# Kernel tuning notes

Hardware: AMD Instinct MI355X
Metric: run time of the kernel (lower is better)

The kernel has to match this reference:

```python
import jax, jax.numpy as jnp
import numpy as np

# dims: batch, seq, model dim, heads, head_k_dim, head_v_dim, conv size
B, S, D, H, DK, DV, K = 1, 2048, 1024, 8, 128, 128, 4
KD, VD = H * DK, H * DV  # key_dim, value_dim


def _silu(x):
    return x * jax.nn.sigmoid(x)


def _l2norm(x, eps=1e-6):
    return x * jax.lax.rsqrt(jnp.sum(x * x, -1, keepdims=True) + eps)


def _causal_conv_silu(x, w):
    # depthwise causal conv1d (ShortConvolution, activation='silu', no bias)
    # x: [b, s, d], w: [d, K]
    Kc = w.shape[1]
    xp = jnp.pad(x, ((0, 0), (Kc - 1, 0), (0, 0)))
    y = sum(xp[:, i:i + x.shape[1], :] * w[:, i] for i in range(Kc))
    return _silu(y)


def _rmsnorm(x, w, eps=1e-5):
    return x * jax.lax.rsqrt(jnp.mean(x * x, -1, keepdims=True) + eps) * w


def _kda(q, k, v, g, beta):
    # gated delta-rule linear attention (KDA), recurrent form == chunk_kda math
    # q,k,g: [B,S,H,DK]; v: [B,S,H,DV]; beta: [B,S,H]
    scale = DK ** -0.5
    qn = _l2norm(q) * scale  # use_qk_l2norm_in_kernel=True
    kn = _l2norm(k)

    def step(Sm, inp):
        q_t, k_t, v_t, g_t, b_t = inp  # [B,H,DK], [B,H,DK], [B,H,DV], [B,H,DK], [B,H]
        Sm = Sm * jnp.exp(g_t)[..., None]                    # per-key-channel decay
        v_new = (v_t - jnp.einsum('bhk,bhkv->bhv', k_t, Sm)) * b_t[..., None]
        Sm = Sm + k_t[..., None] * v_new[..., None, :]       # delta-rule update
        o_t = jnp.einsum('bhk,bhkv->bhv', q_t, Sm)
        return Sm, o_t

    xs = (jnp.swapaxes(qn, 0, 1), jnp.swapaxes(kn, 0, 1), jnp.swapaxes(v, 0, 1),
          jnp.swapaxes(g, 0, 1), jnp.swapaxes(beta, 0, 1))
    S0 = jnp.zeros((q.shape[0], H, DK, DV), jnp.float32)
    _, o = jax.lax.scan(step, S0, xs)
    return jnp.swapaxes(o, 0, 1)  # [B,S,H,DV]


def setup_inputs() -> dict:
    key = jax.random.key(0)
    ks = jax.random.split(key, 20)

    def w(k, shape, fan_in):
        return jax.random.normal(k, shape, jnp.float32) / np.sqrt(fan_in)

    return {
        'x': jax.random.normal(ks[0], (B, S, D), jnp.float32),
        've': jax.random.normal(ks[1], (B, S, D), jnp.float32),
        'sa_lambdas': jax.random.uniform(ks[2], (2,), jnp.float32),
        'Wq': w(ks[3], (KD, D), D), 'Wk': w(ks[4], (KD, D), D), 'Wv': w(ks[5], (VD, D), D),
        'Wo': w(ks[6], (D, VD), VD),
        'wq_conv': w(ks[7], (KD, K), K), 'wk_conv': w(ks[8], (KD, K), K), 'wv_conv': w(ks[9], (VD, K), K),
        'Wf1': w(ks[10], (DV, D), D), 'Wf2': w(ks[11], (KD, DV), DV),
        'Wb': w(ks[12], (H, D), D),
        'A_log': jnp.log(jax.random.uniform(ks[13], (H,), jnp.float32, 1.0, 16.0)),
        'dt_bias': jnp.zeros((KD,), jnp.float32),
        'Wg1': w(ks[14], (DV, D), D), 'Wg2': w(ks[15], (VD, DV), DV),
        'bg2': jnp.zeros((VD,), jnp.float32),
        'w_norm': jnp.ones((DV,), jnp.float32),
    }


def reference(x, ve, sa_lambdas, Wq, Wk, Wv, Wo, wq_conv, wk_conv, wv_conv,
              Wf1, Wf2, Wb, A_log, dt_bias, Wg1, Wg2, bg2, w_norm):
    b, s, _ = x.shape
    # q/k/v projections + short causal conv with silu
    q = _causal_conv_silu(x @ Wq.T, wq_conv)
    k = _causal_conv_silu(x @ Wk.T, wk_conv)
    v = _causal_conv_silu(x @ Wv.T, wv_conv)
    # fused_kda_gate: g = -exp(A_log) * softplus(f_proj(x) + dt_bias), per [H, DK]
    g = (x @ Wf1.T) @ Wf2.T
    g = jax.nn.softplus((g + dt_bias).astype(jnp.float32)).reshape(b, s, H, DK)
    g = -jnp.exp(A_log)[None, None, :, None] * g
    beta = jax.nn.sigmoid((x @ Wb.T).astype(jnp.float32))  # [b,s,H]
    q = q.reshape(b, s, H, DK)
    k = k.reshape(b, s, H, DK)
    v = v.reshape(b, s, H, DV)
    # mix v with value-embedding ve (3-D branch of _mix_v_with_ve)
    ve_v = _causal_conv_silu(ve @ Wv.T, wv_conv).reshape(b, s, H, DV)
    v = sa_lambdas[0] * v + sa_lambdas[1] * ve_v
    o = _kda(q, k, v, g, beta)  # [b,s,H,DV]
    # FusedRMSNormGated(activation='sigmoid'): rmsnorm(o)*w then gate
    g_out = ((x @ Wg1.T) @ Wg2.T + bg2).reshape(b, s, H, DV)
    o = _rmsnorm(o, w_norm) * jax.nn.sigmoid(g_out)
    return o.reshape(b, s, VD) @ Wo.T
```

## Files before the change

kernel.cpp:

```cpp
#include <hip/hip_runtime.h>
#include <math.h>
#include <stdint.h>

#define S_LEN 2048
#define DMODEL 1024
#define NH 8
#define DK_ 128
#define DV_ 128
#define KD_ 1024
#define KCONV 4
#define CW 32
#define NW2 64
#define PREB_STRIDE 17408
#define TKH_OFF 0
#define QHT_OFF 4096
#define KCT_OFF 8192
#define TV_OFF 12288
#define NN_OFF 16384
#define RS 164
#define GS 20

typedef short bf16x8 __attribute__((ext_vector_type(8)));
typedef float f32x4 __attribute__((ext_vector_type(4)));

__device__ __forceinline__ uint16_t f2bf(float f) {
  uint32_t u = __float_as_uint(f);
  u += 0x7FFF + ((u >> 16) & 1);
  return (uint16_t)(u >> 16);
}
__device__ __forceinline__ float bf2f(uint16_t u) {
  return __uint_as_float((uint32_t)u << 16);
}
__device__ __forceinline__ void glds16(const uint16_t* g, uint16_t* l) {
  __builtin_amdgcn_global_load_lds(
      (const __attribute__((address_space(1))) void*)g,
      (__attribute__((address_space(3))) void*)l, 16, 0, 0);
}
__device__ __forceinline__ float dot4(float4 a, float4 b) {
  return fmaf(a.w, b.w, fmaf(a.z, b.z, fmaf(a.y, b.y, a.x * b.x)));
}
__device__ __forceinline__ float4 f4add(float4 a, float4 b) {
  float4 r; r.x = a.x + b.x; r.y = a.y + b.y; r.z = a.z + b.z; r.w = a.w + b.w; return r;
}
__device__ __forceinline__ float4 f4sub(float4 a, float4 b) {
  float4 r; r.x = a.x - b.x; r.y = a.y - b.y; r.z = a.z - b.z; r.w = a.w - b.w; return r;
}
__device__ __forceinline__ float4 f4mul(float4 a, float4 b) {
  float4 r; r.x = a.x * b.x; r.y = a.y * b.y; r.z = a.z * b.z; r.w = a.w * b.w; return r;
}
__device__ __forceinline__ float4 f4s(float4 a, float s) {
  float4 r; r.x = a.x * s; r.y = a.y * s; r.z = a.z * s; r.w = a.w * s; return r;
}
__device__ __forceinline__ float4 f4expc(float4 a) {
  float4 r;
  r.x = expf(fminf(a.x, 0.f)); r.y = expf(fminf(a.y, 0.f));
  r.z = expf(fminf(a.z, 0.f)); r.w = expf(fminf(a.w, 0.f));
  return r;
}
__device__ __forceinline__ float4 f4exp(float4 a) {
  float4 r; r.x = expf(a.x); r.y = expf(a.y); r.z = expf(a.z); r.w = expf(a.w); return r;
}
__device__ __forceinline__ uint4 pack8(float4 a, float4 b) {
  uint4 r;
  r.x = (uint32_t)f2bf(a.x) | ((uint32_t)f2bf(a.y) << 16);
  r.y = (uint32_t)f2bf(a.z) | ((uint32_t)f2bf(a.w) << 16);
  r.z = (uint32_t)f2bf(b.x) | ((uint32_t)f2bf(b.y) << 16);
  r.w = (uint32_t)f2bf(b.z) | ((uint32_t)f2bf(b.w) << 16);
  return r;
}
__device__ __forceinline__ uint2 pack4(f32x4 a) {
  uint2 r;
  r.x = (uint32_t)f2bf(a[0]) | ((uint32_t)f2bf(a[1]) << 16);
  r.y = (uint32_t)f2bf(a[2]) | ((uint32_t)f2bf(a[3]) << 16);
  return r;
}
union U4B8 { uint4 u; bf16x8 b; };
__device__ __forceinline__ bf16x8 u2b(uint4 u) { U4B8 x; x.u = u; return x.b; }

#define DPPADD(x, ctrl) \
  x += __int_as_float(__builtin_amdgcn_update_dpp(0, __float_as_int(x), ctrl, 0xF, 0xF, true))

__device__ __forceinline__ void row8_sum2(float& a, float& b) {
  DPPADD(a, 0xB1); DPPADD(b, 0xB1);
  DPPADD(a, 0x4E); DPPADD(b, 0x4E);
  DPPADD(a, 0x141); DPPADD(b, 0x141);
}
__device__ __forceinline__ void row8_arr8x2(float* x, float* y) {
#pragma unroll
  for (int i = 0; i < 8; i++) { DPPADD(x[i], 0xB1); DPPADD(y[i], 0xB1); }
#pragma unroll
  for (int i = 0; i < 8; i++) { DPPADD(x[i], 0x4E); DPPADD(y[i], 0x4E); }
#pragma unroll
  for (int i = 0; i < 8; i++) { DPPADD(x[i], 0x141); DPPADD(y[i], 0x141); }
}

struct CastArgs {
  const float* s[8];
  uint16_t* d[8];
  int n[8];
};
__global__ __launch_bounds__(256) void cast_multi(CastArgs a) {
  int i = blockIdx.y;
  const int step = gridDim.x * 256 * 8;
  for (int base = (blockIdx.x * 256 + threadIdx.x) * 8; base < a.n[i]; base += step) {
    const float4* sp = (const float4*)(a.s[i] + base);
    float4 x0 = sp[0], x1 = sp[1];
    *(uint4*)(a.d[i] + base) = pack8(x0, x1);
  }
}

__global__ __launch_bounds__(256) void gemm_wc(
    const float* __restrict__ A,
    const float* __restrict__ B,
    uint16_t* __restrict__ C) {
  __shared__ float As[16][68];
  __shared__ float Bs[16][68];
  const int tid = threadIdx.x;
  const int m0 = blockIdx.y * 64, n0 = blockIdx.x * 64;
  const int tx = tid & 15, ty = tid >> 4;
  const int lk = tid & 15, lr = tid >> 4;
  const int bc = tid & 63, bkr = tid >> 6;
  float acc[4][4] = {};
  for (int k0 = 0; k0 < 128; k0 += 16) {
#pragma unroll
    for (int i = 0; i < 4; i++) {
      As[lk][lr + 16 * i] = A[(size_t)(m0 + lr + 16 * i) * 128 + k0 + lk];
      Bs[bkr + 4 * i][bc] = B[(size_t)(k0 + bkr + 4 * i) * 1024 + n0 + bc];
    }
    __syncthreads();
#pragma unroll
    for (int kk = 0; kk < 16; kk++) {
      float4 a4 = *(const float4*)&As[kk][ty * 4];
      float4 b4 = *(const float4*)&Bs[kk][tx * 4];
      float av[4] = {a4.x, a4.y, a4.z, a4.w};
      float bv[4] = {b4.x, b4.y, b4.z, b4.w};
#pragma unroll
      for (int i = 0; i < 4; i++)
#pragma unroll
        for (int jx = 0; jx < 4; jx++) acc[i][jx] = fmaf(av[i], bv[jx], acc[i][jx]);
    }
    __syncthreads();
  }
#pragma unroll
  for (int i = 0; i < 4; i++)
#pragma unroll
    for (int jx = 0; jx < 4; jx++)
      C[(size_t)(m0 + ty * 4 + i) * 1024 + n0 + tx * 4 + jx] = f2bf(acc[i][jx]);
}

__global__ __launch_bounds__(256) void pad_wb(const float* __restrict__ Wb,
                                              uint16_t* __restrict__ Wbp) {
  int idx = blockIdx.x * 256 + threadIdx.x;
  if (idx >= 128 * 1024) return;
  int r = idx >> 10;
  Wbp[idx] = (r < 8) ? f2bf(Wb[idx]) : (uint16_t)0;
}

struct GJobs {
  const uint16_t* A[8];
  const uint16_t* B[8];
  void* C[8];
  int N[8];
  int outbf[8];
};
__global__ __launch_bounds__(256) void gemm_mfma(GJobs j, int K) {
  const int z = blockIdx.z;
  const int N = j.N[z];
  const int n0 = blockIdx.x * 128;
  if (n0 >= N) return;
  __shared__ uint16_t Asb[128 * 32];
  __shared__ uint16_t Bsb[128 * 32];
  const uint16_t* __restrict__ A = j.A[z];
  const uint16_t* __restrict__ B = j.B[z];
  const int tid = threadIdx.x;
  const int w = tid >> 6, lane = tid & 63;
  const int m0 = blockIdx.y * 128;
  const int mw = (w & 1) * 64, nw = (w >> 1) * 64;
  const int c0 = tid, c1 = 256 + tid;
  const int r0 = c0 >> 2, cl0 = (c0 & 3) ^ ((r0 >> 2) & 3);
  const int r1 = c1 >> 2, cl1 = (c1 & 3) ^ ((r1 >> 2) & 3);
  const uint16_t* gA0 = A + (size_t)(m0 + r0) * K + cl0 * 8;
  const uint16_t* gA1 = A + (size_t)(m0 + r1) * K + cl1 * 8;
  const uint16_t* gB0 = B + (size_t)(n0 + r0) * K + cl0 * 8;
  const uint16_t* gB1 = B + (size_t)(n0 + r1) * K + cl1 * 8;
  uint16_t* lA0 = Asb + w * 512;
  uint16_t* lA1 = Asb + 2048 + w * 512;
  uint16_t* lB0 = Bsb + w * 512;
  uint16_t* lB1 = Bsb + 2048 + w * 512;

  const int l15 = lane & 15, q = lane >> 4;
  const int ccq = q ^ ((l15 >> 2) & 3);

  f32x4 acc[4][4] = {};
  for (int k0 = 0; k0 < K; k0 += 32) {
    glds16(gA0 + k0, lA0);
    glds16(gA1 + k0, lA1);
    glds16(gB0 + k0, lB0);
    glds16(gB1 + k0, lB1);
    __syncthreads();
    bf16x8 af[4], bfr[4];
#pragma unroll
    for (int i = 0; i < 4; i++)
      af[i] = *(const bf16x8*)&Asb[(mw + i * 16 + l15) * 32 + ccq * 8];
#pragma unroll
    for (int jx = 0; jx < 4; jx++)
      bfr[jx] = *(const bf16x8*)&Bsb[(nw + jx * 16 + l15) * 32 + ccq * 8];
#pragma unroll
    for (int i = 0; i < 4; i++)
#pragma unroll
      for (int jx = 0; jx < 4; jx++)
        acc[i][jx] = __builtin_amdgcn_mfma_f32_16x16x32_bf16(af[i], bfr[jx],
                                                             acc[i][jx], 0, 0, 0);
    __syncthreads();
  }
  const int obf = j.outbf[z];
#pragma unroll
  for (int i = 0; i < 4; i++) {
#pragma unroll
    for (int jx = 0; jx < 4; jx++) {
      int n = n0 + nw + jx * 16 + l15;
#pragma unroll
      for (int r = 0; r < 4; r++) {
        int m = m0 + mw + i * 16 + q * 4 + r;
        if (obf)
          ((uint16_t*)j.C[z])[(size_t)m * N + n] = f2bf(acc[i][jx][r]);
        else
          ((float*)j.C[z])[(size_t)m * N + n] = acc[i][jx][r];
      }
    }
  }
}

__global__ __launch_bounds__(256) void conv_silu_mix(
    const uint16_t* __restrict__ qp, const uint16_t* __restrict__ kp,
    const uint16_t* __restrict__ vp, const uint16_t* __restrict__ vep,
    const float* __restrict__ wq, const float* __restrict__ wk,
    const float* __restrict__ wv, const float* __restrict__ lam,
    float* __restrict__ qc, float* __restrict__ kc, float* __restrict__ vmx) {
  int idx = blockIdx.x * 256 + threadIdx.x;
  if (idx >= S_LEN * KD_) return;
  int s = idx >> 10, d = idx & 1023;
  float aq = 0.f, ak = 0.f, av = 0.f, ae = 0.f;
#pragma unroll
  for (int i = 0; i < KCONV; i++) {
    int ss = s - (KCONV - 1) + i;
    if (ss < 0) continue;
    size_t off = (size_t)ss * KD_ + d;
    aq = fmaf(bf2f(qp[off]), wq[d * KCONV + i], aq);
    ak = fmaf(bf2f(kp[off]), wk[d * KCONV + i], ak);
    av = fmaf(bf2f(vp[off]), wv[d * KCONV + i], av);
    ae = fmaf(bf2f(vep[off]), wv[d * KCONV + i], ae);
  }
  qc[idx] = aq / (1.f + expf(-aq));
  kc[idx] = ak / (1.f + expf(-ak));
  float sv = av / (1.f + expf(-av));
  float se = ae / (1.f + expf(-ae));
  vmx[idx] = lam[0] * sv + lam[1] * se;
}

__global__ __launch_bounds__(256) void kda_pre(
    const float* __restrict__ qc, const float* __restrict__ kc,
    const float* __restrict__ graw, const float* __restrict__ vm,
    const float* __restrict__ bpre, const float* __restrict__ dt_bias,
    const float* __restrict__ A_log, uint16_t* __restrict__ preB,
    float* __restrict__ preF) {
  __shared__ float kls[32 * RS];
  __shared__ float Gls[32 * RS];
  __shared__ float Mcm[32 * 36];
  __shared__ float bls[32];
  const int w = blockIdx.x >> 3, h = blockIdx.x & 7;
  const int tid = threadIdx.x;
  const int t = tid >> 3, kq = tid & 7;
  const int wv = tid >> 6;
  const size_t gb = (size_t)blockIdx.x * PREB_STRIDE;
  const size_t gf = (size_t)blockIdx.x * 128;

  size_t roff = (size_t)(w * CW + t) * KD_ + h * DK_ + kq * 16;
  float4 kv[4], qv[4], gv[4], dtb[4];
#pragma unroll
  for (int i = 0; i < 4; i++) {
    kv[i] = *(const float4*)(kc + roff + i * 4);
    qv[i] = *(const float4*)(qc + roff + i * 4);
    gv[i] = *(const float4*)(graw + roff + i * 4);
    dtb[i] = *(const float4*)(dt_bias + h * DK_ + kq * 16 + i * 4);
  }
  const float Ahead = expf(A_log[h]);
  if (tid < 32) {
    float b = bpre[(size_t)(w * CW + tid) * 128 + h];
    bls[tid] = 1.f / (1.f + expf(-b));
  }
  float src[32];
  if (tid >= 128) {
    int c2 = tid - 128;
#pragma unroll
    for (int t2 = 0; t2 < 32; t2++)
      src[t2] = vm[(size_t)(w * CW + t2) * KD_ + h * DV_ + c2];
  }
#pragma unroll
  for (int i = 0; i < 4; i++) {
    float vsp[4];
    float xin[4] = {gv[i].x + dtb[i].x, gv[i].y + dtb[i].y,
                    gv[i].z + dtb[i].z, gv[i].w + dtb[i].w};
#pragma unroll
    for (int e = 0; e < 4; e++)
      vsp[e] = (xin[e] > 20.f) ? xin[e] : log1pf(expf(xin[e]));
    gv[i].x = -Ahead * vsp[0]; gv[i].y = -Ahead * vsp[1];
    gv[i].z = -Ahead * vsp[2]; gv[i].w = -Ahead * vsp[3];
  }
  float sk = 0.f, sq = 0.f;
#pragma unroll
  for (int i = 0; i < 4; i++) {
    sk += dot4(kv[i], kv[i]);
    sq += dot4(qv[i], qv[i]);
  }
  row8_sum2(sk, sq);
  float rkn = rsqrtf(sk + 1e-6f);
  float rqn = rsqrtf(sq + 1e-6f) * 0.08838834764831845f;
#pragma unroll
  for (int i = 0; i < 4; i++) {
    kv[i] = f4s(kv[i], rkn);
    qv[i] = f4s(qv[i], rqn);
    *(float4*)&kls[t * RS + kq * GS + i * 4] = kv[i];
    *(float4*)&Gls[t * RS + kq * GS + i * 4] = gv[i];
  }
  __syncthreads();
  float4 Ga[4] = {};
#pragma unroll
  for (int jb = 0; jb < 4; jb++) {
    if (jb <= wv) {
#pragma unroll
      for (int jj = 0; jj < 8; jj++) {
        int j = jb * 8 + jj;
        bool inc = (jb < wv) || (j <= t);
#pragma unroll
        for (int i = 0; i < 4; i++) {
          float4 gj = *(const float4*)&Gls[j * RS + kq * GS + i * 4];
          if (inc) Ga[i] = f4add(Ga[i], gj);
        }
      }
    }
  }
  __syncthreads();
  float4 khr[4];
  float4 Pa[4];
#pragma unroll
  for (int i = 0; i < 4; i++) {
    *(float4*)&Gls[t * RS + kq * GS + i * 4] = Ga[i];
    Pa[i] = f4exp(Ga[i]);
    khr[i] = f4mul(kv[i], Pa[i]);
  }
  {
    float4 q0 = f4mul(qv[0], Pa[0]), q1 = f4mul(qv[1], Pa[1]);
    float4 q2 = f4mul(qv[2], Pa[2]), q3 = f4mul(qv[3], Pa[3]);
    *(uint4*)(preB + gb + QHT_OFF + t * 128 + kq * 16) = pack8(q0, q1);
    *(uint4*)(preB + gb + QHT_OFF + t * 128 + kq * 16 + 8) = pack8(q2, q3);
  }
  if (t == 31) {
#pragma unroll
    for (int i = 0; i < 4; i++)
      *(float4*)(preF + gf + kq * 16 + i * 4) = Pa[i];
  }
  __syncthreads();
#pragma unroll
  for (int i = 0; i < 4; i++) {
    float4 Gfi = *(const float4*)&Gls[31 * RS + kq * GS + i * 4];
    float4 ea = f4expc(f4sub(Gfi, Ga[i]));
    float4 kc4 = f4mul(kv[i], ea);
    float kk[4] = {kc4.x, kc4.y, kc4.z, kc4.w};
#pragma unroll
    for (int e = 0; e < 4; e++)
      preB[gb + KCT_OFF + (kq * 16 + i * 4 + e) * 32 + t] = f2bf(kk[e]);
  }
#pragma unroll
  for (int jb = 0; jb < 4; jb++) {
    if (jb <= wv) {
      float mp8[8], np8[8];
#pragma unroll
      for (int jj = 0; jj < 8; jj++) {
        int j = jb * 8 + jj;
        float m = 0.f, n = 0.f;
#pragma unroll
        for (int i = 0; i < 4; i++) {
          float4 kj = *(const float4*)&kls[j * RS + kq * GS + i * 4];
          float4 Gj = *(const float4*)&Gls[j * RS + kq * GS + i * 4];
          float4 e = f4expc(f4sub(Ga[i], Gj));
          float4 p = f4mul(kj, e);
          m += dot4(kv[i], p);
          n += dot4(qv[i], p);
        }
        mp8[jj] = (j < t) ? m : 0.f;
        np8[jj] = (j <= t) ? n : 0.f;
      }
      row8_arr8x2(mp8, np8);
#pragma unroll
      for (int jj = 0; jj < 8; jj++) {
        if (kq == jj) {
          int j = jb * 8 + jj;
          Mcm[j * 36 + t] = bls[t] * mp8[jj];
          preB[gb + NN_OFF + t * 32 + j] = f2bf(np8[jj]);
        }
      }
    } else {
      preB[gb + NN_OFF + t * 32 + jb * 8 + kq] = 0;
    }
  }
  float bl[32];
#pragma unroll
  for (int i = 0; i < 8; i++) {
    float4 b4 = *(const float4*)&bls[i * 4];
    bl[i * 4 + 0] = b4.x; bl[i * 4 + 1] = b4.y;
    bl[i * 4 + 2] = b4.z; bl[i * 4 + 3] = b4.w;
  }
  __syncthreads();
#pragma unroll
  for (int i = 0; i < 4; i++)
    *(float4*)&kls[t * RS + kq * GS + i * 4] = khr[i];
  __syncthreads();
  if (tid < 128) {
#pragma unroll
    for (int t2 = 0; t2 < 32; t2++)
      src[t2] = kls[t2 * RS + (tid >> 4) * GS + (tid & 15)];
  }
  const int c = tid;
  float acc[32];
#pragma unroll
  for (int i = 0; i < 32; i++) acc[i] = 0.f;
#pragma unroll
  for (int t2 = 0; t2 < 32; t2++) {
    float val = fmaf(bl[t2], src[t2], -acc[t2]);
    if (c < 128)
      preB[gb + TKH_OFF + t2 * 128 + c] = f2bf(val);
    else
      preB[gb + TV_OFF + t2 * 128 + (c - 128)] = f2bf(val);
#pragma unroll
    for (int t3 = t2 + 1; t3 < 32; t3++)
      acc[t3] = fmaf(Mcm[t2 * 36 + t3], val, acc[t3]);
  }
}

__global__ __launch_bounds__(128) void kda_scan(
    const uint16_t* __restrict__ preB, const float* __restrict__ preF,
    float* __restrict__ o) {
  __shared__ uint16_t tkh[2][32 * 136];
  __shared__ uint16_t qht[2][32 * 136];
  __shared__ uint16_t sbf[16 * 136];
  __shared__ uint16_t vbf[16 * 40];
  const int h = blockIdx.x & 7, cg = blockIdx.x >> 3;
  const int tid = threadIdx.x;
  const int wv = tid >> 6, lane = tid & 63;
  const int q = lane >> 4, l15 = lane & 15;

#define SBAR()                          \
  do {                                  \
    __builtin_amdgcn_sched_barrier(0);  \
    __builtin_amdgcn_s_barrier();       \
    __builtin_amdgcn_sched_barrier(0);  \
  } while (0)
#define LGKM0() asm volatile("s_waitcnt lgkmcnt(0)" ::: "memory")

  if (wv == 1) {
    const int row = lane >> 1, half = lane & 1;
    auto sload = [&](uint4 (&a)[8], uint4 (&b)[8], int w) {
      size_t gbs = (size_t)(w * 8 + h) * PREB_STRIDE;
      const uint4* gt = (const uint4*)(preB + gbs + TKH_OFF);
      const uint4* gq = (const uint4*)(preB + gbs + QHT_OFF);
#pragma unroll
      for (int i = 0; i < 8; i++) {
        a[i] = gt[lane * 8 + i];
        b[i] = gq[lane * 8 + i];
      }
    };
    auto swrite = [&](uint4 (&a)[8], uint4 (&b)[8], int buf) {
#pragma unroll
      for (int i = 0; i < 8; i++) {
        *(uint4*)&tkh[buf][row * 136 + half * 64 + i * 8] = a[i];
        *(uint4*)&qht[buf][row * 136 + half * 64 + i * 8] = b[i];
      }
    };
    uint4 aA[8], bA[8], aB[8], bB[8];
    sload(aA, bA, 0);
    sload(aB, bB, 1);
    swrite(aA, bA, 0);
    LGKM0();
    SBAR();
    for (int w = 0; w < NW2; w += 2) {
      if (w + 2 < NW2) sload(aA, bA, w + 2);
      swrite(aB, bB, 1);
      LGKM0();
      SBAR();
      if (w + 3 < NW2) sload(aB, bB, w + 3);
      if (w + 2 < NW2) swrite(aA, bA, 0);
      LGKM0();
      SBAR();
    }
  } else {
    f32x4 s[8] = {};
    auto pload = [&](uint4 (&kct)[8], uint4 (&nrg)[2], float4 (&pb)[8],
                     float (&tvv)[8], int w) {
      const size_t gbs = (size_t)(w * 8 + h) * PREB_STRIDE;
#pragma unroll
      for (int ki = 0; ki < 8; ki++)
        kct[ki] = *(const uint4*)(preB + gbs + KCT_OFF + (16 * ki + l15) * 32 + q * 8);
#pragma unroll
      for (int tt = 0; tt < 2; tt++)
        nrg[tt] = *(const uint4*)(preB + gbs + NN_OFF + (tt * 16 + l15) * 32 + q * 8);
#pragma unroll
      for (int ki = 0; ki < 8; ki++)
        pb[ki] = *(const float4*)(preF + (size_t)(w * 8 + h) * 128 + 16 * ki + q * 4);
#pragma unroll
      for (int tt = 0; tt < 2; tt++)
#pragma unroll
        for (int r = 0; r < 4; r++)
          tvv[tt * 4 + r] =
              bf2f(preB[gbs + TV_OFF + (tt * 16 + q * 4 + r) * 128 + cg * 16 + l15]);
    };
    auto compute = [&](uint4 (&kct)[8], uint4 (&nrg)[2], float4 (&pb)[8],
                       float (&tvv)[8], int buf, int w) {
#pragma unroll
      for (int ki = 0; ki < 8; ki++)
        *(uint2*)&sbf[l15 * 136 + 16 * ki + q * 4] = pack4(s[ki]);
      f32x4 aat[2] = {}, bbt[2] = {};
#pragma unroll
      for (int kc = 0; kc < 4; kc++) {
        bf16x8 bS = *(const bf16x8*)&sbf[l15 * 136 + kc * 32 + q * 8];
#pragma unroll
        for (int tt = 0; tt < 2; tt++) {
          bf16x8 aT = *(const bf16x8*)&tkh[buf][(tt * 16 + l15) * 136 + kc * 32 + q * 8];
          bf16x8 aQ = *(const bf16x8*)&qht[buf][(tt * 16 + l15) * 136 + kc * 32 + q * 8];
          aat[tt] = __builtin_amdgcn_mfma_f32_16x16x32_bf16(aT, bS, aat[tt], 0, 0, 0);
          bbt[tt] = __builtin_amdgcn_mfma_f32_16x16x32_bf16(aQ, bS, bbt[tt], 0, 0, 0);
        }
      }
#pragma unroll
      for (int tt = 0; tt < 2; tt++) {
        f32x4 vn;
#pragma unroll
        for (int r = 0; r < 4; r++) vn[r] = tvv[tt * 4 + r] - aat[tt][r];
        *(uint2*)&vbf[l15 * 40 + tt * 16 + q * 4] = pack4(vn);
      }
      bf16x8 bV = *(const bf16x8*)&vbf[l15 * 40 + q * 8];
#pragma unroll
      for (int tt = 0; tt < 2; tt++) {
        f32x4 ot = __builtin_amdgcn_mfma_f32_16x16x32_bf16(u2b(nrg[tt]), bV,
                                                           bbt[tt], 0, 0, 0);
#pragma unroll
        for (int r = 0; r < 4; r++)
          o[(size_t)(w * CW + tt * 16 + q * 4 + r) * KD_ + h * DK_ + cg * 16 + l15] =
              ot[r];
      }
#pragma unroll
      for (int ki = 0; ki < 8; ki++) {
#pragma unroll
        for (int r = 0; r < 4; r++) s[ki][r] *= pb[ki][r];
        s[ki] = __builtin_amdgcn_mfma_f32_16x16x32_bf16(u2b(kct[ki]), bV, s[ki], 0, 0, 0);
      }
    };
    uint4 kA[8], nA[2]; float4 pA[8]; float tA[8];
    uint4 kB[8], nB[2]; float4 pB[8]; float tB[8];
    pload(kA, nA, pA, tA, 0);
    pload(kB, nB, pB, tB, 1);
    SBAR();
    for (int w = 0; w < NW2; w += 2) {
      compute(kA, nA, pA, tA, 0, w);
      if (w + 2 < NW2) pload(kA, nA, pA, tA, w + 2);
      SBAR();
      compute(kB, nB, pB, tB, 1, w + 1);
      if (w + 3 < NW2) pload(kB, nB, pB, tB, w + 3);
      SBAR();
    }
  }
#undef SBAR
#undef LGKM0
}

__global__ __launch_bounds__(64) void gated_rmsnorm(
    const float* __restrict__ o, const float* __restrict__ g2raw,
    const float* __restrict__ bg2, const float* __restrict__ wn,
    uint16_t* __restrict__ ob) {
  size_t base = (size_t)blockIdx.x * DV_;
  int t = threadIdx.x;
  float a = o[base + t], b = o[base + t + 64];
  float ss = a * a + b * b;
#pragma unroll
  for (int off = 32; off > 0; off >>= 1) ss += __shfl_xor(ss, off);
  float r = rsqrtf(ss * (1.f / 128.f) + 1e-5f);
  int c0 = (int)((base + t) & 1023), c1 = (int)((base + t + 64) & 1023);
  float ga = 1.f / (1.f + expf(-(g2raw[base + t] + bg2[c0])));
  float gb = 1.f / (1.f + expf(-(g2raw[base + t + 64] + bg2[c1])));
  ob[base + t] = f2bf(a * r * wn[t] * ga);
  ob[base + t + 64] = f2bf(b * r * wn[t + 64] * gb);
}

extern "C" void kernel_launch(void* const* d_in, const int* in_sizes, int n_in,
                              void* d_out, int out_size, void* d_ws, size_t ws_size,
                              hipStream_t stream) {
  const float* x = (const float*)d_in[0];
  const float* ve = (const float*)d_in[1];
  const float* lam = (const float*)d_in[2];
  const float* Wq = (const float*)d_in[3];
  const float* Wk = (const float*)d_in[4];
  const float* Wv = (const float*)d_in[5];
  const float* Wo = (const float*)d_in[6];
  const float* wq_conv = (const float*)d_in[7];
  const float* wk_conv = (const float*)d_in[8];
  const float* wv_conv = (const float*)d_in[9];
  const float* Wf1 = (const float*)d_in[10];
  const float* Wf2 = (const float*)d_in[11];
  const float* Wb = (const float*)d_in[12];
  const float* A_log = (const float*)d_in[13];
  const float* dt_bias = (const float*)d_in[14];
  const float* Wg1 = (const float*)d_in[15];
  const float* Wg2 = (const float*)d_in[16];
  const float* bg2 = (const float*)d_in[17];
  const float* w_norm = (const float*)d_in[18];
  float* out = (float*)d_out;

  float* ws = (float*)d_ws;
  const size_t SZ = (size_t)S_LEN * KD_;
  uint16_t* qpb = (uint16_t*)ws;
  uint16_t* kpb = (uint16_t*)(ws + SZ / 2);
  uint16_t* vpb = (uint16_t*)(ws + SZ);
  uint16_t* vepb = (uint16_t*)(ws + 3 * SZ / 2);
  float* q_c = ws + 2 * SZ;
  float* k_c = ws + 3 * SZ;
  float* v_mix = ws + 4 * SZ;
  float* graw = ws + 5 * SZ;
  float* o_buf = graw;
  float* g2raw = k_c;
  uint16_t* bws = (uint16_t*)(ws + 6 * SZ);
  uint16_t* xb = bws;
  uint16_t* veb = xb + SZ;
  uint16_t* Wqb = veb + SZ;
  uint16_t* Wkb = Wqb + (size_t)KD_ * DMODEL;
  uint16_t* Wvb = Wkb + (size_t)KD_ * DMODEL;
  uint16_t* Wob = Wvb + (size_t)KD_ * DMODEL;
  uint16_t* Wg1b = Wob + (size_t)DMODEL * KD_;
  uint16_t* Wg2b = Wg1b + (size_t)DV_ * DMODEL;
  uint16_t* Wcb = Wg2b + (size_t)KD_ * DV_;
  uint16_t* Wbp = Wcb + (size_t)KD_ * DMODEL;
  uint16_t* g1b = Wbp + (size_t)128 * 1024;
  uint16_t* ob = g1b + (size_t)S_LEN * DV_;
  float* bpre2 = ws + 18 * (size_t)1024 * 1024;
  float* preF = ws + (size_t)20 * 1024 * 1024;
  uint16_t* preB = (uint16_t*)(ws + (size_t)20 * 1024 * 1024 + 65536 + 64);

  dim3 blk(256);
  int ew_blocks = (S_LEN * KD_ + 255) / 256;

  CastArgs ca;
  ca.s[0] = x;   ca.d[0] = xb;   ca.n[0] = S_LEN * DMODEL;
  ca.s[1] = ve;  ca.d[1] = veb;  ca.n[1] = S_LEN * DMODEL;
  ca.s[2] = Wq;  ca.d[2] = Wqb;  ca.n[2] = KD_ * DMODEL;
  ca.s[3] = Wk;  ca.d[3] = Wkb;  ca.n[3] = KD_ * DMODEL;
  ca.s[4] = Wv;  ca.d[4] = Wvb;  ca.n[4] = KD_ * DMODEL;
  ca.s[5] = Wo;  ca.d[5] = Wob;  ca.n[5] = DMODEL * KD_;
  ca.s[6] = Wg1; ca.d[6] = Wg1b; ca.n[6] = DV_ * DMODEL;
  ca.s[7] = Wg2; ca.d[7] = Wg2b; ca.n[7] = KD_ * DV_;
  cast_multi<<<dim3(256, 8), blk, 0, stream>>>(ca);

  gemm_wc<<<dim3(16, 16), blk, 0, stream>>>(Wf2, Wf1, Wcb);
  pad_wb<<<dim3(512), blk, 0, stream>>>(Wb, Wbp);

  GJobs jq;
  jq.A[0] = xb;  jq.B[0] = Wqb;  jq.C[0] = qpb;   jq.N[0] = KD_; jq.outbf[0] = 1;
  jq.A[1] = xb;  jq.B[1] = Wkb;  jq.C[1] = kpb;   jq.N[1] = KD_; jq.outbf[1] = 1;
  jq.A[2] = xb;  jq.B[2] = Wvb;  jq.C[2] = vpb;   jq.N[2] = KD_; jq.outbf[2] = 1;
  jq.A[3] = veb; jq.B[3] = Wvb;  jq.C[3] = vepb;  jq.N[3] = KD_; jq.outbf[3] = 1;
  jq.A[4] = xb;  jq.B[4] = Wg1b; jq.C[4] = g1b;   jq.N[4] = DV_; jq.outbf[4] = 1;
  jq.A[5] = xb;  jq.B[5] = Wcb;  jq.C[5] = graw;  jq.N[5] = KD_; jq.outbf[5] = 0;
  jq.A[6] = xb;  jq.B[6] = Wbp;  jq.C[6] = bpre2; jq.N[6] = 128; jq.outbf[6] = 0;
  gemm_mfma<<<dim3(8, 16, 7), blk, 0, stream>>>(jq, DMODEL);

  conv_silu_mix<<<ew_blocks, blk, 0, stream>>>(qpb, kpb, vpb, vepb,
                                               wq_conv, wk_conv, wv_conv, lam,
                                               q_c, k_c, v_mix);

  kda_pre<<<dim3(NW2 * 8), blk, 0, stream>>>(q_c, k_c, graw, v_mix, bpre2,
                                             dt_bias, A_log, preB, preF);
  kda_scan<<<dim3(64), dim3(128), 0, stream>>>(preB, preF, o_buf);

  GJobs jg2;
  jg2.A[0] = g1b; jg2.B[0] = Wg2b; jg2.C[0] = g2raw; jg2.N[0] = KD_; jg2.outbf[0] = 0;
  gemm_mfma<<<dim3(8, 16, 1), blk, 0, stream>>>(jg2, DV_);

  gated_rmsnorm<<<dim3(S_LEN * NH), dim3(64), 0, stream>>>(o_buf, g2raw, bg2,
                                                           w_norm, ob);

  GJobs jo;
  jo.A[0] = ob; jo.B[0] = Wob; jo.C[0] = out; jo.N[0] = DMODEL; jo.outbf[0] = 0;
  gemm_mfma<<<dim3(8, 16, 1), blk, 0, stream>>>(jo, KD_);
}
```

Before: 420.4 us.

## Use direct global-to-LDS loads with triple-buffered swizzled tiles in kda_scan

The loader wave in kda_scan now issues direct global-to-LDS loads (glds16) into a three-slot ring of XOR-swizzled tiles instead of staging through registers and writing padded LDS rows. Completion is tracked with vmcnt waits rather than lgkmcnt, and compute reads with the matching swizzle. The aim is to cut loader-wave register traffic and VALU/LDS write work, and to let the next chunk's loads stay in flight across a barrier. The risk is a race if the vmcnt accounting or ring-slot reuse is wrong. It also depends on the glds16 helper, which is defined in a part of the file not shown.

Measured after the change: 397.3 us. 5.5% less time.

```diff
diff --git a/kernel.cpp b/kernel.cpp
--- a/kernel.cpp
+++ b/kernel.cpp
@@ -438,16 +438,16 @@
   }
 }
 
-__global__ __launch_bounds__(128) void kda_scan(
+__global__ __launch_bounds__(128, 1) void kda_scan(
     const uint16_t* __restrict__ preB, const float* __restrict__ preF,
     float* __restrict__ o) {
-  __shared__ uint16_t tkh[2][32 * 136];
-  __shared__ uint16_t qht[2][32 * 136];
+  __shared__ uint16_t tkh3[3 * 32 * 128];
+  __shared__ uint16_t qht3[3 * 32 * 128];
   __shared__ uint16_t sbf[16 * 136];
   __shared__ uint16_t vbf[16 * 40];
   const int h = blockIdx.x & 7, cg = blockIdx.x >> 3;
   const int tid = threadIdx.x;
-  const int wv = tid >> 6, lane = tid & 63;
+  const int wvi = tid >> 6, lane = tid & 63;
   const int q = lane >> 4, l15 = lane & 15;
 
 #define SBAR()                          \
@@ -456,41 +456,37 @@
     __builtin_amdgcn_s_barrier();       \
     __builtin_amdgcn_sched_barrier(0);  \
   } while (0)
-#define LGKM0() asm volatile("s_waitcnt lgkmcnt(0)" ::: "memory")
-
-  if (wv == 1) {
-    const int row = lane >> 1, half = lane & 1;
-    auto sload = [&](uint4 (&a)[8], uint4 (&b)[8], int w) {
+#define WAITV(n)                                            \
+  do {                                                      \
+    asm volatile("s_waitcnt vmcnt(" #n ")" ::: "memory");   \
+    __builtin_amdgcn_sched_barrier(0);                      \
+  } while (0)
+
+  if (wvi == 1) {
+    auto sissue = [&](int w, int b3) {
       size_t gbs = (size_t)(w * 8 + h) * PREB_STRIDE;
-      const uint4* gt = (const uint4*)(preB + gbs + TKH_OFF);
-      const uint4* gq = (const uint4*)(preB + gbs + QHT_OFF);
+      const uint16_t* gt = preB + gbs + TKH_OFF;
+      const uint16_t* gq = preB + gbs + QHT_OFF;
+      uint16_t* lt = tkh3 + b3 * 4096;
+      uint16_t* lq = qht3 + b3 * 4096;
 #pragma unroll
       for (int i = 0; i < 8; i++) {
-        a[i] = gt[lane * 8 + i];
-        b[i] = gq[lane * 8 + i];
+        int row = i * 4 + (lane >> 4);
+        int sl = (lane & 15) ^ (row & 7);
+        glds16(gt + row * 128 + sl * 8, lt + i * 512);
+        glds16(gq + row * 128 + sl * 8, lq + i * 512);
       }
     };
-    auto swrite = [&](uint4 (&a)[8], uint4 (&b)[8], int buf) {
-#pragma unroll
-      for (int i = 0; i < 8; i++) {
-        *(uint4*)&tkh[buf][row * 136 + half * 64 + i * 8] = a[i];
-        *(uint4*)&qht[buf][row * 136 + half * 64 + i * 8] = b[i];
-      }
-    };
-    uint4 aA[8], bA[8], aB[8], bB[8];
-    sload(aA, bA, 0);
-    sload(aB, bB, 1);
-    swrite(aA, bA, 0);
-    LGKM0();
+    sissue(0, 0);
+    sissue(1, 1);
+    WAITV(16);
     SBAR();
     for (int w = 0; w < NW2; w += 2) {
-      if (w + 2 < NW2) sload(aA, bA, w + 2);
-      swrite(aB, bB, 1);
-      LGKM0();
+      if (w + 2 < NW2) { sissue(w + 2, (w + 2) % 3); WAITV(16); }
+      else             { WAITV(0); }
       SBAR();
-      if (w + 3 < NW2) sload(aB, bB, w + 3);
-      if (w + 2 < NW2) swrite(aA, bA, 0);
-      LGKM0();
+      if (w + 3 < NW2) { sissue(w + 3, (w + 3) % 3); WAITV(16); }
+      else             { WAITV(0); }
       SBAR();
     }
   } else {
@@ -515,7 +511,9 @@
               bf2f(preB[gbs + TV_OFF + (tt * 16 + q * 4 + r) * 128 + cg * 16 + l15]);
     };
     auto compute = [&](uint4 (&kct)[8], uint4 (&nrg)[2], float4 (&pb)[8],
-                       float (&tvv)[8], int buf, int w) {
+                       float (&tvv)[8], int b3, int w) {
+      const uint16_t* tb = tkh3 + b3 * 4096;
+      const uint16_t* qb = qht3 + b3 * 4096;
 #pragma unroll
       for (int ki = 0; ki < 8; ki++)
         *(uint2*)&sbf[l15 * 136 + 16 * ki + q * 4] = pack4(s[ki]);
@@ -525,8 +523,10 @@
         bf16x8 bS = *(const bf16x8*)&sbf[l15 * 136 + kc * 32 + q * 8];
 #pragma unroll
         for (int tt = 0; tt < 2; tt++) {
-          bf16x8 aT = *(const bf16x8*)&tkh[buf][(tt * 16 + l15) * 136 + kc * 32 + q * 8];
-          bf16x8 aQ = *(const bf16x8*)&qht[buf][(tt * 16 + l15) * 136 + kc * 32 + q * 8];
+          int row = tt * 16 + l15;
+          int sl = (kc * 4 + q) ^ (l15 & 7);
+          bf16x8 aT = *(const bf16x8*)&tb[row * 128 + sl * 8];
+          bf16x8 aQ = *(const bf16x8*)&qb[row * 128 + sl * 8];
           aat[tt] = __builtin_amdgcn_mfma_f32_16x16x32_bf16(aT, bS, aat[tt], 0, 0, 0);
           bbt[tt] = __builtin_amdgcn_mfma_f32_16x16x32_bf16(aQ, bS, bbt[tt], 0, 0, 0);
         }
@@ -561,16 +561,16 @@
     pload(kB, nB, pB, tB, 1);
     SBAR();
     for (int w = 0; w < NW2; w += 2) {
-      compute(kA, nA, pA, tA, 0, w);
+      compute(kA, nA, pA, tA, w % 3, w);
       if (w + 2 < NW2) pload(kA, nA, pA, tA, w + 2);
       SBAR();
-      compute(kB, nB, pB, tB, 1, w + 1);
+      compute(kB, nB, pB, tB, (w + 1) % 3, w + 1);
       if (w + 3 < NW2) pload(kB, nB, pB, tB, w + 3);
       SBAR();
     }
   }
 #undef SBAR
-#undef LGKM0
+#undef WAITV
 }
 
 __global__ __launch_bounds__(64) void gated_rmsnorm(
```
